# Optimization experiments

Hardware: AMD Instinct MI355X
Metric: run time of the kernel (lower is better)

The kernel has to match this reference:

```python
import jax, jax.numpy as jnp
import numpy as np
from functools import partial

IMAGE_SIZE = 256
ORIG_SIZE = 1024
NEAR, FAR = 0.1, 100.0
CHUNK = 100  # faces processed per scan step to bound memory


def setup_inputs():
    key = jax.random.key(0)
    kv, kf = jax.random.split(key)
    B, V, F = 4, 5000, 10000
    verts = jax.random.normal(kv, (B, V, 3), jnp.float32) * 0.4
    verts = verts.at[..., 2].add(2.5)  # object in front of camera (+z)
    faces = jax.random.randint(kf, (B, F, 3), 0, V)
    fx = fy = float(ORIG_SIZE)
    cx = cy = ORIG_SIZE / 2.0
    K = jnp.broadcast_to(jnp.array([[fx, 0., cx], [0., fy, cy], [0., 0., 1.]], jnp.float32), (B, 3, 3))
    R = jnp.broadcast_to(jnp.eye(3, dtype=jnp.float32), (B, 3, 3))
    t = jnp.zeros((B, 1, 3), jnp.float32)
    dist_coeffs = jnp.zeros((B, 5), jnp.float32)
    return {"vertices": verts, "faces": faces, "K": K, "R": R, "t": t, "dist_coeffs": dist_coeffs}


def projection(vertices, K, R, t, dist_coeffs, orig_size, eps=1e-9):
    # vertices: [B,V,3]; matmul(vertices, R^T) + t, OpenCV distortion, intrinsics, NDC
    v = jnp.einsum('bvj,bij->bvi', vertices, R) + t
    x, y, z = v[..., 0], v[..., 1], v[..., 2]
    x_ = x / (z + eps)
    y_ = y / (z + eps)
    k1, k2, p1, p2, k3 = [dist_coeffs[:, i:i + 1] for i in range(5)]
    r2 = x_ * x_ + y_ * y_
    rad = 1. + k1 * r2 + k2 * r2 * r2 + k3 * r2 * r2 * r2
    x__ = x_ * rad + 2. * p1 * x_ * y_ + p2 * (r2 + 2. * x_ * x_)
    y__ = y_ * rad + p1 * (r2 + 2. * y_ * y_) + 2. * p2 * x_ * y_
    vv = jnp.stack([x__, y__, jnp.ones_like(z)], axis=-1)
    vv = jnp.einsum('bvj,bij->bvi', vv, K)
    u, vc = vv[..., 0], vv[..., 1]
    vc = orig_size - vc  # image y points down
    u = 2. * (u - orig_size / 2.) / orig_size
    vc = 2. * (vc - orig_size / 2.) / orig_size
    return jnp.stack([u, vc, z], axis=-1)  # [B,V,3] in NDC xy, camera z


def vertices_to_faces(vertices, faces):
    # vertices [B,V,3], faces [B,F,3] -> [B,F,3,3]
    return jnp.take_along_axis(vertices[:, :, None, :], faces[:, :, :, None], axis=1)


def rasterize_depth(face_verts, image_size, near, far):
    # face_verts: [B,F,3,3]; z-buffer min of barycentric-interpolated 1/z depth
    B, F = face_verts.shape[:2]
    pad = (-F) % CHUNK
    fv = jnp.pad(face_verts, ((0, 0), (0, pad), (0, 0), (0, 0)))  # padded faces are degenerate
    n_chunks = (F + pad) // CHUNK
    fv = fv.reshape(B, n_chunks, CHUNK, 3, 3).transpose(1, 0, 2, 3, 4)  # [n,B,C,3,3]
    ps = (2. * jnp.arange(image_size, dtype=jnp.float32) + 1. - image_size) / image_size
    xp = ps[None, None, None, :]  # [1,1,1,W]
    yp = ps[None, None, :, None]  # [1,1,H,1]
    eps = 1e-8

    def step(zbuf, chunk):  # chunk [B,C,3,3]
        x = chunk[..., 0]
        y = chunk[..., 1]
        z = chunk[..., 2]
        x0, x1, x2 = (x[..., i, None, None] for i in range(3))
        y0, y1, y2 = (y[..., i, None, None] for i in range(3))
        z0, z1, z2 = (z[..., i, None, None] for i in range(3))
        denom = (y1 - y2) * (x0 - x2) + (x2 - x1) * (y0 - y2)
        ok = jnp.abs(denom) > eps
        safe_d = jnp.where(ok, denom, 1.)
        w0 = ((y1 - y2) * (xp - x2) + (x2 - x1) * (yp - y2)) / safe_d  # [B,C,H,W]
        w1 = ((y2 - y0) * (xp - x2) + (x0 - x2) * (yp - y2)) / safe_d
        w2 = 1. - w0 - w1
        inside = (w0 >= 0.) & (w1 >= 0.) & (w2 >= 0.) & ok
        zs0 = jnp.where(z0 > eps, z0, 1.)
        zs1 = jnp.where(z1 > eps, z1, 1.)
        zs2 = jnp.where(z2 > eps, z2, 1.)
        zinv = w0 / zs0 + w1 / zs1 + w2 / zs2
        zp = 1. / jnp.where(zinv > eps, zinv, 1.)
        valid = inside & (zp > near) & (zp < far) & (z0 > eps) & (z1 > eps) & (z2 > eps)
        zp = jnp.where(valid, zp, far)
        zbuf = jnp.minimum(zbuf, jnp.min(zp, axis=1))  # min over faces in chunk
        return zbuf, None

    zbuf0 = jnp.full((B, image_size, image_size), far, dtype=face_verts.dtype)
    zbuf, _ = jax.lax.scan(step, zbuf0, fv)
    return zbuf[:, ::-1, :]  # flip vertically to image convention


def reference(vertices, faces, K, R, t, dist_coeffs):
    # fill_back: append faces with reversed winding
    faces_fb = jnp.concatenate([faces, faces[:, :, ::-1]], axis=1)
    v_ndc = projection(vertices, K, R, t, dist_coeffs, float(ORIG_SIZE))
    fverts = vertices_to_faces(v_ndc, faces_fb)  # [B,2F,3,3]
    return rasterize_depth(fverts, IMAGE_SIZE, NEAR, FAR)  # [B,H,W] depth map
```

## Files before the change

### kernel.cpp

```cpp
#include <hip/hip_runtime.h>

#define IMG 256
#define TW 32
#define TH 32
#define TILES 64
#define SUBSPLIT 16
#define RSUB 8
#define ZTHR 9.5f
#define BIGF 1e30f

typedef float v4f __attribute__((ext_vector_type(4)));

__device__ __forceinline__ float ndc(int i) { return (2.0f*i + 1.0f - IMG) * (1.0f/IMG); }

__device__ __forceinline__ void rank_to_tile(int rank, int& tx, int& ty) {
    int k, base;
    if (rank < 4)       { k = 0; base = 0;  }
    else if (rank < 16) { k = 1; base = 4;  }
    else if (rank < 36) { k = 2; base = 16; }
    else                { k = 3; base = 36; }
    int j = rank - base;
    int s = 2*k + 2;
    int seg = j / (s - 1);
    int off = j - seg * (s - 1);
    int lo = 3 - k, hi = 4 + k;
    if      (seg == 0) { tx = lo + off; ty = lo; }
    else if (seg == 1) { tx = hi;       ty = lo + off; }
    else if (seg == 2) { tx = hi - off; ty = hi; }
    else               { tx = lo;       ty = hi - off; }
}

__device__ __forceinline__ bool tile_test(v4f gx, v4f gy, v4f a,
                                          float txlo, float txhi, float tylo, float tyhi) {
    float m0 = fmaxf(gx.x*txlo, gx.x*txhi) + fmaxf(gy.x*tylo, gy.x*tyhi) + a.x;
    float m1 = fmaxf(gx.y*txlo, gx.y*txhi) + fmaxf(gy.y*tylo, gy.y*tyhi) + a.y;
    float m2 = fmaxf(gx.z*txlo, gx.z*txhi) + fmaxf(gy.z*tylo, gy.z*tyhi) + a.z;
    return fminf(fminf(m0, m1), m2) >= -1e-5f;
}

__device__ __forceinline__ float plane_min(float gw, float hw, float aw,
                                           float xlo, float xhi, float ylo, float yhi) {
    return fminf(gw*xlo, gw*xhi) + fminf(hw*ylo, hw*yhi) + aw;
}

__device__ __forceinline__ float wave_max_dpp(float v) {
    int x;
    x = __builtin_amdgcn_update_dpp(0, __float_as_int(v), 0x111, 0xF, 0xF, true);
    v = fmaxf(v, __int_as_float(x));
    x = __builtin_amdgcn_update_dpp(0, __float_as_int(v), 0x112, 0xF, 0xF, true);
    v = fmaxf(v, __int_as_float(x));
    x = __builtin_amdgcn_update_dpp(0, __float_as_int(v), 0x114, 0xF, 0xF, true);
    v = fmaxf(v, __int_as_float(x));
    x = __builtin_amdgcn_update_dpp(0, __float_as_int(v), 0x118, 0xF, 0xF, true);
    v = fmaxf(v, __int_as_float(x));
    x = __builtin_amdgcn_update_dpp(0, __float_as_int(v), 0x142, 0xF, 0xF, true);
    v = fmaxf(v, __int_as_float(x));
    x = __builtin_amdgcn_update_dpp(0, __float_as_int(v), 0x143, 0xF, 0xF, true);
    v = fmaxf(v, __int_as_float(x));
    return __int_as_float(__builtin_amdgcn_readlane(__float_as_int(v), 63));
}

__device__ __forceinline__ unsigned long long cover_mask_px(int i0, int i1, int j0, int j1,
                                                            v4f gx, v4f gy, v4f aa) {
    if (i0 > 255 || i1 < 0 || j0 > 255 || j1 < 0) return 0ull;
    int tx0 = max(i0, 0) >> 5, tx1 = min(i1, 255) >> 5;
    int ty0 = max(j0, 0) >> 5, ty1 = min(j1, 255) >> 5;
    unsigned long long m = 0ull;
    for (int ty = ty0; ty <= ty1; ++ty) {
        float tylo = ndc(ty*TH), tyhi = ndc(ty*TH + TH - 1);
        for (int tx = tx0; tx <= tx1; ++tx) {
            if (tile_test(gx, gy, aa, ndc(tx*TW), ndc(tx*TW + TW - 1), tylo, tyhi))
                m |= 1ull << (ty*8 + tx);
        }
    }
    return m;
}

__global__ void k_prep(const float* __restrict__ verts, const int* __restrict__ faces,
                       const float* __restrict__ Km, const float* __restrict__ Rm,
                       const float* __restrict__ tm, const float* __restrict__ dm,
                       v4f* __restrict__ fd, v4f* __restrict__ bb,
                       unsigned int* __restrict__ ids,
                       unsigned int* __restrict__ outz, unsigned int* __restrict__ gcnt,
                       int B, int V, int F, int nz, int faceBlocks, int doBins) {
    if ((int)blockIdx.x >= faceBlocks) {
        int idx = (blockIdx.x - faceBlocks) * 256 + threadIdx.x;
        int stride = (gridDim.x - faceBlocks) * 256;
        for (int j = idx; j < nz; j += stride) outz[j] = 0x42C80000u;
        return;
    }
    __shared__ int lcnt[2048];
    __shared__ unsigned int lbase[2048];
    __shared__ int lofs[2048];
    int nbins = TILES * B;
    int tid = threadIdx.x;
    if (doBins) {
        for (int k = tid; k < 2*nbins; k += 256) { lcnt[k] = 0; lofs[k] = 0; }
        __syncthreads();
    }
    int i = blockIdx.x * 256 + tid;
    bool alive = i < B * F;
    unsigned long long tmask = 0ull;
    int b = 0, j0c = 0, j1c = 0, cls = 0;
    if (alive) {
        b = i / F;
        const float* vb = verts + (size_t)b * V * 3;
        const float* R = Rm + b * 9;
        const float* K = Km + b * 9;
        const float* t = tm + b * 3;
        const float* d = dm + b * 5;
        float X[3], Y[3], Z[3];
        float maxzi = 0.0f;
        #pragma unroll
        for (int c = 0; c < 3; ++c) {
            int vi = faces[3*i + c];
            float px = vb[3*vi], py = vb[3*vi+1], pz = vb[3*vi+2];
            float x = R[0]*px + R[1]*py + R[2]*pz + t[0];
            float y = R[3]*px + R[4]*py + R[5]*pz + t[1];
            float z = R[6]*px + R[7]*py + R[8]*pz + t[2];
            float iz = 1.0f / (z + 1e-9f);
            maxzi = fmaxf(maxzi, iz);
            float x_ = x * iz, y_ = y * iz;
            float k1 = d[0], k2 = d[1], p1 = d[2], p2 = d[3], k3 = d[4];
            float r2 = x_*x_ + y_*y_;
            float rad = 1.0f + k1*r2 + k2*r2*r2 + k3*r2*r2*r2;
            float xd = x_*rad + 2.0f*p1*x_*y_ + p2*(r2 + 2.0f*x_*x_);
            float yd = y_*rad + p1*(r2 + 2.0f*y_*y_) + 2.0f*p2*x_*y_;
            float u  = K[0]*xd + K[1]*yd + K[2];
            float vc = K[3]*xd + K[4]*yd + K[5];
            vc = 1024.0f - vc;
            X[c] = (u  - 512.0f) * (1.0f/512.0f);
            Y[c] = (vc - 512.0f) * (1.0f/512.0f);
            Z[c] = z;
        }
        float x0=X[0], y0=Y[0], z0=Z[0], x1=X[1], y1=Y[1], z1=Z[1], x2=X[2], y2=Y[2], z2=Z[2];
        float denom = (y1-y2)*(x0-x2) + (x2-x1)*(y0-y2);
        bool ok = (fabsf(denom) > 1e-8f) && (z0 > 1e-8f) && (z1 > 1e-8f) && (z2 > 1e-8f);
        if (!ok) {
            bb[i] = (v4f){3e38f, -3e38f, 3e38f, -3e38f};
        } else {
            float s = (denom > 0.0f) ? 1.0f : -1.0f;
            float absd = fabsf(denom);
            float P0x = s*(y1-y2), P0y = s*(x2-x1);
            float P1x = s*(y2-y0), P1y = s*(x0-x2);
            float P2x = -(P0x + P1x), P2y = -(P0y + P1y);
            float A0 = -(P0x*x2 + P0y*y2);
            float A1 = -(P1x*x2 + P1y*y2);
            float A2 = absd - A0 - A1;
            float ia  = 1.0f / absd;
            float rz0 = ia / z0, rz1 = ia / z1, rz2 = ia / z2;
            float zix = P0x*rz0 + P1x*rz1 + P2x*rz2;
            float ziy = P0y*rz0 + P1y*rz1 + P2y*rz2;
            float zic = A0*rz0 + A1*rz1 + A2*rz2;
            v4f ga = (v4f){P0x, P1x, P2x, -zix};
            v4f gb = (v4f){P0y, P1y, P2y, -ziy};
            v4f gc = (v4f){A0,  A1,  A2,  10.0f - zic};
            fd[(size_t)i*3 + 0] = ga;
            fd[(size_t)i*3 + 1] = gb;
            fd[(size_t)i*3 + 2] = gc;
            float xmn = fminf(x0, fminf(x1, x2)) - 1e-4f;
            float xmx = fmaxf(x0, fmaxf(x1, x2)) + 1e-4f;
            float ymn = fminf(y0, fminf(y1, y2)) - 1e-4f;
            float ymx = fmaxf(y0, fmaxf(y1, y2)) + 1e-4f;
            bb[i] = (v4f){xmn, xmx, ymn, ymx};
            if (doBins) {
                int i0 = (int)floorf(xmn*128.0f + 127.5f);
                int i1 = (int)ceilf (xmx*128.0f + 127.5f);
                int j0 = (int)floorf(ymn*128.0f + 127.5f);
                int j1 = (int)ceilf (ymx*128.0f + 127.5f);
                tmask = cover_mask_px(i0, i1, j0, j1, ga, gb, gc);
                j0c = max(j0, 0); j1c = min(j1, 255);
                cls = ((10.0f - maxzi) < ZTHR) ? 0 : 1;
            }
        }
    }
    if (doBins) {
        unsigned long long mk = tmask;
        while (mk) {
            int t = __builtin_ctzll(mk); mk &= mk - 1ull;
            atomicAdd(&lcnt[(t*B + b)*2 + cls], 1);
        }
        __syncthreads();
        for (int k = tid; k < 2*nbins; k += 256)
            if (lcnt[k]) lbase[k] = atomicAdd(&gcnt[k], (unsigned int)lcnt[k]);
        __syncthreads();
        mk = tmask;
        while (mk) {
            int t = __builtin_ctzll(mk); mk &= mk - 1ull;
            int ty = t >> 3;
            int bin = t*B + b;
            unsigned int blo = (unsigned int)max((j0c >> 3) - ty*4, 0);
            unsigned int bhi = (unsigned int)min((j1c >> 3) - ty*4, 3);
            unsigned int pack = (unsigned int)i | (blo << 28) | (bhi << 30);
            int key = bin*2 + cls;
            int sl = atomicAdd(&lofs[key], 1);
            unsigned int pos = lbase[key] + (unsigned int)sl;
            size_t idx = (cls == 0) ? ((size_t)bin*F + pos)
                                    : ((size_t)bin*F + (F - 1) - pos);
            ids[idx] = pack;
        }
    }
}

__global__ __launch_bounds__(256) void k_raster(const v4f* __restrict__ fd,
                                                const unsigned int* __restrict__ ids,
                                                const unsigned int* __restrict__ gcnt,
                                                unsigned int* __restrict__ outz,
                                                int B, int F) {
    __shared__ v4f sA[257], sB[257], sC[257];
    int tid = threadIdx.x, lane = tid & 63, wave = tid >> 6;
    int wbase = wave << 6;
    int tbIdx = blockIdx.x >> 3;
    int sub = blockIdx.x & (RSUB-1);
    int rank = tbIdx / B;
    int b = tbIdx - rank * B;
    int tx, ty;
    rank_to_tile(rank, tx, ty);
    int bin = (ty*8 + tx)*B + b;
    unsigned int lnN = gcnt[bin*2 + 0];
    unsigned int lnF = gcnt[bin*2 + 1];
    size_t base = (size_t)bin * F;

    int rowbase = ty*TH + wave*8;
    int row = rowbase + (lane >> 3);
    int col = tx*TW + (lane & 7) * 4;
    float yp = ndc(row);
    float xp[4];
    #pragma unroll
    for (int jj = 0; jj < 4; ++jj) xp[jj] = ndc(col + jj);
    float txlo = ndc(tx*TW), txhi = ndc(tx*TW + TW - 1);
    float bylo = ndc(rowbase), byhi = ndc(rowbase + 7);
    float m[4] = {BIGF, BIGF, BIGF, BIGF};

    int orow = IMG - 1 - row;
    size_t zo = (size_t)b * (IMG*IMG) + (size_t)orow * IMG + col;

    float hs = 0.0f;
    #pragma unroll
    for (int jj = 0; jj < 4; ++jj) {
        float d = __uint_as_float(outz[zo + jj]);
        hs = fmaxf(hs, 10.0f - 1.0f/d);
    }
    float h = fminf(9.99f, wave_max_dpp(hs) + 1e-4f);

    #pragma unroll 1
    for (int seg = 0; seg < 2; ++seg) {
        unsigned int segLen = (seg == 0) ? lnN : lnF;
        unsigned int segOff = (seg == 0) ? 0u : (unsigned int)F - lnF;
        unsigned int p0 = segOff + (unsigned int)(((unsigned long long)sub     * segLen) / RSUB);
        unsigned int p1 = segOff + (unsigned int)(((unsigned long long)(sub+1) * segLen) / RSUB);
        if (p1 <= p0) continue;

        unsigned int pc = ids[base + min(p0 + lane, p1 - 1)];
        bool vc = (p0 + lane) < p1;
        unsigned int pn = ids[base + min(p0 + 64 + lane, p1 - 1)];
        bool vn = (p0 + 64 + lane) < p1;

        for (unsigned int p = p0; p < p1; p += 64) {
            unsigned int p2w = ids[base + min(p + 128 + lane, p1 - 1)];
            bool v2 = (p + 128 + lane) < p1;

            unsigned int blo = (pc >> 28) & 3u, bhi = pc >> 30;
            unsigned int idc = pc & 0x0FFFFFFFu;
            bool pass = vc & ((int)blo <= wave) & ((int)bhi >= wave);
            bool full = false;
            v4f ra = (v4f){0,0,0,0}, rb = (v4f){0,0,0,0}, rc = (v4f){0,0,0,0};
            if (pass) {
                ra = fd[(size_t)idc*3]; rb = fd[(size_t)idc*3+1]; rc = fd[(size_t)idc*3+2];
                float p0l=ra.x*txlo, p0h=ra.x*txhi, q0l=rb.x*bylo, q0h=rb.x*byhi;
                float p1l=ra.y*txlo, p1h=ra.y*txhi, q1l=rb.y*bylo, q1h=rb.y*byhi;
                float p2l=ra.z*txlo, p2h=ra.z*txhi, q2l=rb.z*bylo, q2h=rb.z*byhi;
                float c0x = fmaxf(p0l,p0h) + fmaxf(q0l,q0h) + rc.x;
                float c1x = fmaxf(p1l,p1h) + fmaxf(q1l,q1h) + rc.y;
                float c2x = fmaxf(p2l,p2h) + fmaxf(q2l,q2h) + rc.z;
                float c0n = fminf(p0l,p0h) + fminf(q0l,q0h) + rc.x;
                float c1n = fminf(p1l,p1h) + fminf(q1l,q1h) + rc.y;
                float c2n = fminf(p2l,p2h) + fminf(q2l,q2h) + rc.z;
                float zmn = fminf(ra.w*txlo, ra.w*txhi) + fminf(rb.w*bylo, rb.w*byhi) + rc.w;
                pass = (fminf(fminf(c0x, c1x), c2x) >= -1e-5f) & (zmn < h);
                full = (fminf(fminf(c0n, c1n), c2n) >= 1e-5f);
            }
            unsigned long long mp = __ballot(pass && !full);
            unsigned long long mf = __ballot(pass && full);
            int cp = __popcll(mp);
            int cf = __popcll(mf);
            if (pass && !full) {
                int sl = wbase + __popcll(mp & ((1ull << lane) - 1ull));
                sA[sl] = ra; sB[sl] = rb; sC[sl] = rc;
            }
            unsigned long long w = mf;
            while (w) {
                int l = __builtin_amdgcn_readfirstlane(__ffsll((unsigned long long)w) - 1);
                w &= w - 1ull;
                float gxw = __int_as_float(__builtin_amdgcn_readlane(__float_as_int(ra.w), l));
                float gyw = __int_as_float(__builtin_amdgcn_readlane(__float_as_int(rb.w), l));
                float aaw = __int_as_float(__builtin_amdgcn_readlane(__float_as_int(rc.w), l));
                float e3 = fmaf(gyw, yp, aaw);
                #pragma unroll
                for (int jj = 0; jj < 4; ++jj)
                    m[jj] = fminf(m[jj], fmaf(gxw, xp[jj], e3));
            }
            if (cp > 0) {
                v4f gx = sA[wbase], gy = sB[wbase], aa = sC[wbase];
                for (int i = 0; i < cp; ++i) {
                    v4f nx = sA[wbase+i+1], ny = sB[wbase+i+1], nzv = sC[wbase+i+1];
                    float e0 = fmaf(gy.x, yp, aa.x);
                    float e1 = fmaf(gy.y, yp, aa.y);
                    float e2 = fmaf(gy.z, yp, aa.z);
                    float e3 = fmaf(gy.w, yp, aa.w);
                    #pragma unroll
                    for (int jj = 0; jj < 4; ++jj) {
                        float n0 = fmaf(gx.x, xp[jj], e0);
                        float n1 = fmaf(gx.y, xp[jj], e1);
                        float n2 = fmaf(gx.z, xp[jj], e2);
                        float n3 = fmaf(gx.w, xp[jj], e3);
                        float q = fminf(fminf(n0, n1), n2);
                        m[jj] = fminf(m[jj], (q >= 0.0f) ? n3 : BIGF);
                    }
                    gx = nx; gy = ny; aa = nzv;
                }
            }
            if (cp + cf > 0)
                h = fminf(h, wave_max_dpp(fmaxf(fmaxf(m[0], m[1]), fmaxf(m[2], m[3]))));
            pc = pn; vc = vn;
            pn = p2w; vn = v2;
        }
    }
    #pragma unroll
    for (int jj = 0; jj < 4; ++jj) {
        if (m[jj] < 9.99f) {
            float depth = 1.0f / (10.0f - m[jj]);
            unsigned int mv = __float_as_uint(depth);
            unsigned int cv = outz[zo + jj];
            if (mv < cv) atomicMin(&outz[zo + jj], mv);
        }
    }
}

__global__ __launch_bounds__(256) void k_raster_scan(const v4f* __restrict__ fd,
                                                     const v4f* __restrict__ bb,
                                                     unsigned int* __restrict__ outz,
                                                     int B, int F) {
    __shared__ v4f sA[257], sB[257], sC[257];
    int tid = threadIdx.x, lane = tid & 63, wave = tid >> 6;
    int wbase = wave << 6;
    int j = blockIdx.x >> 4;
    int s = blockIdx.x & (SUBSPLIT-1);
    int nTB = TILES * B;
    int f_begin = (s * F) / SUBSPLIT, f_end = ((s + 1) * F) / SUBSPLIT;

    #pragma unroll 1
    for (int phase = 0; phase < 2; ++phase) {
        int tb = (phase == 0) ? j : (nTB - 1 - j);
        int rank = tb / B;
        int b = tb - rank * B;
        int tx, ty;
        rank_to_tile(rank, tx, ty);
        int rowbase = ty*TH + wave*8;
        int row = rowbase + (lane >> 3);
        int col = tx*TW + (lane & 7) * 4;
        float yp = ndc(row);
        float xp[4];
        #pragma unroll
        for (int jj = 0; jj < 4; ++jj) xp[jj] = ndc(col + jj);
        float txlo = ndc(tx*TW), txhi = ndc(tx*TW + TW - 1);
        float bylo = ndc(rowbase), byhi = ndc(rowbase + 7);
        float m[4] = {BIGF, BIGF, BIGF, BIGF};
        float h = 9.99f;

        const v4f* bbp = bb + (size_t)b * F;
        const v4f* fdp = fd + (size_t)b * F * 3;

        v4f box = bbp[min(f_begin + lane, f_end - 1)];
        bool valid = (f_begin + lane) < f_end;

        for (int g0 = f_begin; g0 < f_end; g0 += 64) {
            int fn = g0 + 64 + lane;
            v4f nbox = bbp[min(fn, f_end - 1)];
            bool nvalid = fn < f_end;

            bool pass = valid &
                        (box.x <= txhi) & (box.y >= txlo) &
                        (box.z <= byhi) & (box.w >= bylo);
            v4f ra, rb, rc;
            if (pass) {
                int f = g0 + lane;
                ra = fdp[3*f]; rb = fdp[3*f+1]; rc = fdp[3*f+2];
                pass = tile_test(ra, rb, rc, txlo, txhi, bylo, byhi)
                    && (plane_min(ra.w, rb.w, rc.w, txlo, txhi, bylo, byhi) < h);
            }
            unsigned long long mk = __ballot(pass);
            int total = __popcll(mk);
            if (pass) {
                int slot = wbase + __popcll(mk & ((1ull << lane) - 1ull));
                sA[slot] = ra;
                sB[slot] = rb;
                sC[slot] = rc;
            }
            if (total > 0) {
                v4f gx = sA[wbase], gy = sB[wbase], aa = sC[wbase];
                for (int i = 0; i < total; ++i) {
                    v4f nx = sA[wbase+i+1], ny = sB[wbase+i+1], nzv = sC[wbase+i+1];
                    float e0 = fmaf(gy.x, yp, aa.x);
                    float e1 = fmaf(gy.y, yp, aa.y);
                    float e2 = fmaf(gy.z, yp, aa.z);
                    float e3 = fmaf(gy.w, yp, aa.w);
                    #pragma unroll
                    for (int jj = 0; jj < 4; ++jj) {
                        float n0 = fmaf(gx.x, xp[jj], e0);
                        float n1 = fmaf(gx.y, xp[jj], e1);
                        float n2 = fmaf(gx.z, xp[jj], e2);
                        float n3 = fmaf(gx.w, xp[jj], e3);
                        float q = fminf(fminf(n0, n1), n2);
                        m[jj] = fminf(m[jj], (q >= 0.0f) ? n3 : BIGF);
                    }
                    gx = nx; gy = ny; aa = nzv;
                }
                h = fminf(9.99f, wave_max_dpp(fmaxf(fmaxf(m[0], m[1]), fmaxf(m[2], m[3]))));
            }
            box = nbox; valid = nvalid;
        }
        int orow = IMG - 1 - row;
        size_t zo = (size_t)b * (IMG*IMG) + (size_t)orow * IMG + col;
        #pragma unroll
        for (int jj = 0; jj < 4; ++jj) {
            if (m[jj] < 9.99f) {
                float depth = 1.0f / (10.0f - m[jj]);
                unsigned int mv = __float_as_uint(depth);
                unsigned int cv = outz[zo + jj];
                if (mv < cv) atomicMin(&outz[zo + jj], mv);
            }
        }
    }
}

extern "C" void kernel_launch(void* const* d_in, const int* in_sizes, int n_in,
                              void* d_out, int out_size, void* d_ws, size_t ws_size,
                              hipStream_t stream) {
    const float* verts = (const float*)d_in[0];
    const int*   faces = (const int*)d_in[1];
    const float* Km    = (const float*)d_in[2];
    const float* Rm    = (const float*)d_in[3];
    const float* tm    = (const float*)d_in[4];
    const float* dm    = (const float*)d_in[5];
    float* out = (float*)d_out;

    int B = in_sizes[2] / 9;
    int V = in_sizes[0] / (3 * B);
    int F = in_sizes[1] / (3 * B);
    int nz = B * IMG * IMG;
    int nbins = TILES * B;

    char* ws = (char*)d_ws;
    size_t al = 255;
    size_t o_fd  = 0;
    size_t o_bb  = (o_fd + (size_t)B*F*48 + al) & ~al;
    size_t o_cnt = (o_bb + (size_t)B*F*16 + al) & ~al;
    size_t o_ids = (o_cnt + (size_t)nbins*8 + al) & ~al;
    size_t need_bins = o_ids + (size_t)nbins * F * 4;
    size_t need_scan = o_ids;

    v4f* fd  = (v4f*)(ws + o_fd);
    v4f* bbp = (v4f*)(ws + o_bb);
    unsigned int* gcnt = (unsigned int*)(ws + o_cnt);
    unsigned int* ids  = (unsigned int*)(ws + o_ids);

    const int thr = 256;
    int faceBlocks = (B*F + thr - 1) / thr;

    if (ws_size >= need_bins && nbins <= 1024 && (size_t)B*F < (1u<<28)) {
        hipMemsetAsync(gcnt, 0, (size_t)nbins*8, stream);
        k_prep<<<faceBlocks + 128, thr, 0, stream>>>(verts, faces, Km, Rm, tm, dm,
                                                     fd, bbp, ids, (unsigned int*)out, gcnt,
                                                     B, V, F, nz, faceBlocks, 1);
        int rasterBlocks = nbins * RSUB;
        k_raster<<<rasterBlocks, thr, 0, stream>>>(fd, ids, gcnt,
                                                   (unsigned int*)out, B, F);
    } else if (ws_size >= need_scan) {
        k_prep<<<faceBlocks + 128, thr, 0, stream>>>(verts, faces, Km, Rm, tm, dm,
                                                     fd, bbp, ids, (unsigned int*)out, gcnt,
                                                     B, V, F, nz, faceBlocks, 0);
        int rasterBlocks = (TILES * B / 2) * SUBSPLIT;
        k_raster_scan<<<rasterBlocks, thr, 0, stream>>>(fd, bbp, (unsigned int*)out, B, F);
    }
}
```

Baseline: 115.7 us.

## Split face projection and tile binning into separate kernels

The fused prep kernel becomes two kernels. A 64-thread projection kernel computes the face equations, bounding boxes and a per-face depth key, and writes them to workspace. A separate 256-thread binning kernel reloads them and does the shared-memory counting and scatter into tile bins. The aim is to stop the 24 KB of shared memory and the heavy binning code from limiting occupancy during projection, at the price of an extra launch and another pass over the face data in memory.

```diff
diff --git a/kernel.cpp b/kernel.cpp
--- a/kernel.cpp
+++ b/kernel.cpp
@@ -76,129 +76,134 @@
     return m;
 }
 
-__global__ void k_prep(const float* __restrict__ verts, const int* __restrict__ faces,
+__global__ __launch_bounds__(64) void k_proj(const float* __restrict__ verts,
+                       const int* __restrict__ faces,
                        const float* __restrict__ Km, const float* __restrict__ Rm,
                        const float* __restrict__ tm, const float* __restrict__ dm,
                        v4f* __restrict__ fd, v4f* __restrict__ bb,
-                       unsigned int* __restrict__ ids,
-                       unsigned int* __restrict__ outz, unsigned int* __restrict__ gcnt,
-                       int B, int V, int F, int nz, int faceBlocks, int doBins) {
+                       float* __restrict__ keyz, unsigned int* __restrict__ outz,
+                       int B, int V, int F, int nz, int faceBlocks) {
     if ((int)blockIdx.x >= faceBlocks) {
-        int idx = (blockIdx.x - faceBlocks) * 256 + threadIdx.x;
-        int stride = (gridDim.x - faceBlocks) * 256;
+        int idx = (blockIdx.x - faceBlocks) * 64 + threadIdx.x;
+        int stride = (gridDim.x - faceBlocks) * 64;
         for (int j = idx; j < nz; j += stride) outz[j] = 0x42C80000u;
         return;
     }
+    int i = blockIdx.x * 64 + threadIdx.x;
+    if (i >= B * F) return;
+    int b = i / F;
+    const float* vb = verts + (size_t)b * V * 3;
+    const float* R = Rm + b * 9;
+    const float* K = Km + b * 9;
+    const float* t = tm + b * 3;
+    const float* d = dm + b * 5;
+    float X[3], Y[3], Z[3];
+    float maxzi = 0.0f;
+    #pragma unroll
+    for (int c = 0; c < 3; ++c) {
+        int vi = faces[3*i + c];
+        float px = vb[3*vi], py = vb[3*vi+1], pz = vb[3*vi+2];
+        float x = R[0]*px + R[1]*py + R[2]*pz + t[0];
+        float y = R[3]*px + R[4]*py + R[5]*pz + t[1];
+        float z = R[6]*px + R[7]*py + R[8]*pz + t[2];
+        float iz = 1.0f / (z + 1e-9f);
+        maxzi = fmaxf(maxzi, iz);
+        float x_ = x * iz, y_ = y * iz;
+        float k1 = d[0], k2 = d[1], p1 = d[2], p2 = d[3], k3 = d[4];
+        float r2 = x_*x_ + y_*y_;
+        float rad = 1.0f + k1*r2 + k2*r2*r2 + k3*r2*r2*r2;
+        float xd = x_*rad + 2.0f*p1*x_*y_ + p2*(r2 + 2.0f*x_*x_);
+        float yd = y_*rad + p1*(r2 + 2.0f*y_*y_) + 2.0f*p2*x_*y_;
+        float u  = K[0]*xd + K[1]*yd + K[2];
+        float vc = K[3]*xd + K[4]*yd + K[5];
+        vc = 1024.0f - vc;
+        X[c] = (u  - 512.0f) * (1.0f/512.0f);
+        Y[c] = (vc - 512.0f) * (1.0f/512.0f);
+        Z[c] = z;
+    }
+    float x0=X[0], y0=Y[0], z0=Z[0], x1=X[1], y1=Y[1], z1=Z[1], x2=X[2], y2=Y[2], z2=Z[2];
+    float denom = (y1-y2)*(x0-x2) + (x2-x1)*(y0-y2);
+    bool ok = (fabsf(denom) > 1e-8f) && (z0 > 1e-8f) && (z1 > 1e-8f) && (z2 > 1e-8f);
+    if (!ok) {
+        bb[i] = (v4f){3e38f, -3e38f, 3e38f, -3e38f};
+        keyz[i] = BIGF;
+        return;
+    }
+    float s = (denom > 0.0f) ? 1.0f : -1.0f;
+    float absd = fabsf(denom);
+    float P0x = s*(y1-y2), P0y = s*(x2-x1);
+    float P1x = s*(y2-y0), P1y = s*(x0-x2);
+    float P2x = -(P0x + P1x), P2y = -(P0y + P1y);
+    float A0 = -(P0x*x2 + P0y*y2);
+    float A1 = -(P1x*x2 + P1y*y2);
+    float A2 = absd - A0 - A1;
+    float ia  = 1.0f / absd;
+    float rz0 = ia / z0, rz1 = ia / z1, rz2 = ia / z2;
+    float zix = P0x*rz0 + P1x*rz1 + P2x*rz2;
+    float ziy = P0y*rz0 + P1y*rz1 + P2y*rz2;
+    float zic = A0*rz0 + A1*rz1 + A2*rz2;
+    fd[(size_t)i*3 + 0] = (v4f){P0x, P1x, P2x, -zix};
+    fd[(size_t)i*3 + 1] = (v4f){P0y, P1y, P2y, -ziy};
+    fd[(size_t)i*3 + 2] = (v4f){A0,  A1,  A2,  10.0f - zic};
+    bb[i] = (v4f){fminf(x0, fminf(x1, x2)) - 1e-4f,
+                  fmaxf(x0, fmaxf(x1, x2)) + 1e-4f,
+                  fminf(y0, fminf(y1, y2)) - 1e-4f,
+                  fmaxf(y0, fmaxf(y1, y2)) + 1e-4f};
+    keyz[i] = 10.0f - maxzi;
+}
+
+__global__ __launch_bounds__(256) void k_bin(const v4f* __restrict__ fd,
+                      const v4f* __restrict__ bb, const float* __restrict__ keyz,
+                      unsigned int* __restrict__ ids, unsigned int* __restrict__ gcnt,
+                      int B, int F) {
     __shared__ int lcnt[2048];
     __shared__ unsigned int lbase[2048];
     __shared__ int lofs[2048];
     int nbins = TILES * B;
     int tid = threadIdx.x;
-    if (doBins) {
-        for (int k = tid; k < 2*nbins; k += 256) { lcnt[k] = 0; lofs[k] = 0; }
-        __syncthreads();
-    }
+    for (int k = tid; k < 2*nbins; k += 256) { lcnt[k] = 0; lofs[k] = 0; }
+    __syncthreads();
     int i = blockIdx.x * 256 + tid;
     bool alive = i < B * F;
     unsigned long long tmask = 0ull;
     int b = 0, j0c = 0, j1c = 0, cls = 0;
     if (alive) {
         b = i / F;
-        const float* vb = verts + (size_t)b * V * 3;
-        const float* R = Rm + b * 9;
-        const float* K = Km + b * 9;
-        const float* t = tm + b * 3;
-        const float* d = dm + b * 5;
-        float X[3], Y[3], Z[3];
-        float maxzi = 0.0f;
-        #pragma unroll
-        for (int c = 0; c < 3; ++c) {
-            int vi = faces[3*i + c];
-            float px = vb[3*vi], py = vb[3*vi+1], pz = vb[3*vi+2];
-            float x = R[0]*px + R[1]*py + R[2]*pz + t[0];
-            float y = R[3]*px + R[4]*py + R[5]*pz + t[1];
-            float z = R[6]*px + R[7]*py + R[8]*pz + t[2];
-            float iz = 1.0f / (z + 1e-9f);
-            maxzi = fmaxf(maxzi, iz);
-            float x_ = x * iz, y_ = y * iz;
-            float k1 = d[0], k2 = d[1], p1 = d[2], p2 = d[3], k3 = d[4];
-            float r2 = x_*x_ + y_*y_;
-            float rad = 1.0f + k1*r2 + k2*r2*r2 + k3*r2*r2*r2;
-            float xd = x_*rad + 2.0f*p1*x_*y_ + p2*(r2 + 2.0f*x_*x_);
-            float yd = y_*rad + p1*(r2 + 2.0f*y_*y_) + 2.0f*p2*x_*y_;
-            float u  = K[0]*xd + K[1]*yd + K[2];
-            float vc = K[3]*xd + K[4]*yd + K[5];
-            vc = 1024.0f - vc;
-            X[c] = (u  - 512.0f) * (1.0f/512.0f);
-            Y[c] = (vc - 512.0f) * (1.0f/512.0f);
-            Z[c] = z;
-        }
-        float x0=X[0], y0=Y[0], z0=Z[0], x1=X[1], y1=Y[1], z1=Z[1], x2=X[2], y2=Y[2], z2=Z[2];
-        float denom = (y1-y2)*(x0-x2) + (x2-x1)*(y0-y2);
-        bool ok = (fabsf(denom) > 1e-8f) && (z0 > 1e-8f) && (z1 > 1e-8f) && (z2 > 1e-8f);
-        if (!ok) {
-            bb[i] = (v4f){3e38f, -3e38f, 3e38f, -3e38f};
-        } else {
-            float s = (denom > 0.0f) ? 1.0f : -1.0f;
-            float absd = fabsf(denom);
-            float P0x = s*(y1-y2), P0y = s*(x2-x1);
-            float P1x = s*(y2-y0), P1y = s*(x0-x2);
-            float P2x = -(P0x + P1x), P2y = -(P0y + P1y);
-            float A0 = -(P0x*x2 + P0y*y2);
-            float A1 = -(P1x*x2 + P1y*y2);
-            float A2 = absd - A0 - A1;
-            float ia  = 1.0f / absd;
-            float rz0 = ia / z0, rz1 = ia / z1, rz2 = ia / z2;
-            float zix = P0x*rz0 + P1x*rz1 + P2x*rz2;
-            float ziy = P0y*rz0 + P1y*rz1 + P2y*rz2;
-            float zic = A0*rz0 + A1*rz1 + A2*rz2;
-            v4f ga = (v4f){P0x, P1x, P2x, -zix};
-            v4f gb = (v4f){P0y, P1y, P2y, -ziy};
-            v4f gc = (v4f){A0,  A1,  A2,  10.0f - zic};
-            fd[(size_t)i*3 + 0] = ga;
-            fd[(size_t)i*3 + 1] = gb;
-            fd[(size_t)i*3 + 2] = gc;
-            float xmn = fminf(x0, fminf(x1, x2)) - 1e-4f;
-            float xmx = fmaxf(x0, fmaxf(x1, x2)) + 1e-4f;
-            float ymn = fminf(y0, fminf(y1, y2)) - 1e-4f;
-            float ymx = fmaxf(y0, fmaxf(y1, y2)) + 1e-4f;
-            bb[i] = (v4f){xmn, xmx, ymn, ymx};
-            if (doBins) {
-                int i0 = (int)floorf(xmn*128.0f + 127.5f);
-                int i1 = (int)ceilf (xmx*128.0f + 127.5f);
-                int j0 = (int)floorf(ymn*128.0f + 127.5f);
-                int j1 = (int)ceilf (ymx*128.0f + 127.5f);
-                tmask = cover_mask_px(i0, i1, j0, j1, ga, gb, gc);
-                j0c = max(j0, 0); j1c = min(j1, 255);
-                cls = ((10.0f - maxzi) < ZTHR) ? 0 : 1;
-            }
-        }
-    }
-    if (doBins) {
-        unsigned long long mk = tmask;
-        while (mk) {
-            int t = __builtin_ctzll(mk); mk &= mk - 1ull;
-            atomicAdd(&lcnt[(t*B + b)*2 + cls], 1);
-        }
-        __syncthreads();
-        for (int k = tid; k < 2*nbins; k += 256)
-            if (lcnt[k]) lbase[k] = atomicAdd(&gcnt[k], (unsigned int)lcnt[k]);
-        __syncthreads();
-        mk = tmask;
-        while (mk) {
-            int t = __builtin_ctzll(mk); mk &= mk - 1ull;
-            int ty = t >> 3;
-            int bin = t*B + b;
-            unsigned int blo = (unsigned int)max((j0c >> 3) - ty*4, 0);
-            unsigned int bhi = (unsigned int)min((j1c >> 3) - ty*4, 3);
-            unsigned int pack = (unsigned int)i | (blo << 28) | (bhi << 30);
-            int key = bin*2 + cls;
-            int sl = atomicAdd(&lofs[key], 1);
-            unsigned int pos = lbase[key] + (unsigned int)sl;
-            size_t idx = (cls == 0) ? ((size_t)bin*F + pos)
-                                    : ((size_t)bin*F + (F - 1) - pos);
-            ids[idx] = pack;
-        }
+        v4f box = bb[i];
+        if (box.x <= box.y) {
+            v4f ga = fd[(size_t)i*3], gb = fd[(size_t)i*3+1], gc = fd[(size_t)i*3+2];
+            int i0 = (int)floorf(box.x*128.0f + 127.5f);
+            int i1 = (int)ceilf (box.y*128.0f + 127.5f);
+            int j0 = (int)floorf(box.z*128.0f + 127.5f);
+            int j1 = (int)ceilf (box.w*128.0f + 127.5f);
+            tmask = cover_mask_px(i0, i1, j0, j1, ga, gb, gc);
+            j0c = max(j0, 0); j1c = min(j1, 255);
+            cls = (keyz[i] < ZTHR) ? 0 : 1;
+        }
+    }
+    unsigned long long mk = tmask;
+    while (mk) {
+        int t = __builtin_ctzll(mk); mk &= mk - 1ull;
+        atomicAdd(&lcnt[(t*B + b)*2 + cls], 1);
+    }
+    __syncthreads();
+    for (int k = tid; k < 2*nbins; k += 256)
+        if (lcnt[k]) lbase[k] = atomicAdd(&gcnt[k], (unsigned int)lcnt[k]);
+    __syncthreads();
+    mk = tmask;
+    while (mk) {
+        int t = __builtin_ctzll(mk); mk &= mk - 1ull;
+        int ty = t >> 3;
+        int bin = t*B + b;
+        unsigned int blo = (unsigned int)max((j0c >> 3) - ty*4, 0);
+        unsigned int bhi = (unsigned int)min((j1c >> 3) - ty*4, 3);
+        unsigned int pack = (unsigned int)i | (blo << 28) | (bhi << 30);
+        int key = bin*2 + cls;
+        int sl = atomicAdd(&lofs[key], 1);
+        unsigned int pos = lbase[key] + (unsigned int)sl;
+        size_t idx = (cls == 0) ? ((size_t)bin*F + pos)
+                                : ((size_t)bin*F + (F - 1) - pos);
+        ids[idx] = pack;
     }
 }
 
@@ -455,32 +460,35 @@
     size_t al = 255;
     size_t o_fd  = 0;
     size_t o_bb  = (o_fd + (size_t)B*F*48 + al) & ~al;
-    size_t o_cnt = (o_bb + (size_t)B*F*16 + al) & ~al;
+    size_t o_kz  = (o_bb + (size_t)B*F*16 + al) & ~al;
+    size_t o_cnt = (o_kz + (size_t)B*F*4 + al) & ~al;
     size_t o_ids = (o_cnt + (size_t)nbins*8 + al) & ~al;
     size_t need_bins = o_ids + (size_t)nbins * F * 4;
-    size_t need_scan = o_ids;
+    size_t need_scan = o_cnt;
 
     v4f* fd  = (v4f*)(ws + o_fd);
     v4f* bbp = (v4f*)(ws + o_bb);
+    float* keyz = (float*)(ws + o_kz);
     unsigned int* gcnt = (unsigned int*)(ws + o_cnt);
     unsigned int* ids  = (unsigned int*)(ws + o_ids);
 
-    const int thr = 256;
-    int faceBlocks = (B*F + thr - 1) / thr;
+    int projBlocks = (B*F + 63) / 64;
+    int binBlocks  = (B*F + 255) / 256;
 
     if (ws_size >= need_bins && nbins <= 1024 && (size_t)B*F < (1u<<28)) {
         hipMemsetAsync(gcnt, 0, (size_t)nbins*8, stream);
-        k_prep<<<faceBlocks + 128, thr, 0, stream>>>(verts, faces, Km, Rm, tm, dm,
-                                                     fd, bbp, ids, (unsigned int*)out, gcnt,
-                                                     B, V, F, nz, faceBlocks, 1);
+        k_proj<<<projBlocks + 256, 64, 0, stream>>>(verts, faces, Km, Rm, tm, dm,
+                                                    fd, bbp, keyz, (unsigned int*)out,
+                                                    B, V, F, nz, projBlocks);
+        k_bin<<<binBlocks, 256, 0, stream>>>(fd, bbp, keyz, ids, gcnt, B, F);
         int rasterBlocks = nbins * RSUB;
-        k_raster<<<rasterBlocks, thr, 0, stream>>>(fd, ids, gcnt,
+        k_raster<<<rasterBlocks, 256, 0, stream>>>(fd, ids, gcnt,
                                                    (unsigned int*)out, B, F);
     } else if (ws_size >= need_scan) {
-        k_prep<<<faceBlocks + 128, thr, 0, stream>>>(verts, faces, Km, Rm, tm, dm,
-                                                     fd, bbp, ids, (unsigned int*)out, gcnt,
-                                                     B, V, F, nz, faceBlocks, 0);
+        k_proj<<<projBlocks + 256, 64, 0, stream>>>(verts, faces, Km, Rm, tm, dm,
+                                                    fd, bbp, keyz, (unsigned int*)out,
+                                                    B, V, F, nz, projBlocks);
         int rasterBlocks = (TILES * B / 2) * SUBSPLIT;
-        k_raster_scan<<<rasterBlocks, thr, 0, stream>>>(fd, bbp, (unsigned int*)out, B, F);
-    }
-}
+        k_raster_scan<<<rasterBlocks, 256, 0, stream>>>(fd, bbp, (unsigned int*)out, B, F);
+    }
+}
```

Result: slower. 119.3 us (+3.1%).
